# Kernel tuning notes

Hardware: AMD Instinct MI355X
Metric: run time of the kernel (lower is better)

## Reference

```python
import jax, jax.numpy as jnp
import numpy as np

B, A, N_OBS, HX, N_ACT = 8192, 32, 128, 64, 16

def setup_inputs() -> dict:
    key = jax.random.key(0)
    ks = jax.random.split(key, 12)
    s = lambda *shape: 0.05 * jax.random.normal(ks[setup_inputs.i], shape, dtype=jnp.float32)
    out = {}
    setup_inputs.i = 0
    def nxt(*shape):
        setup_inputs.i += 1
        return 0.05 * jax.random.normal(ks[setup_inputs.i], shape, dtype=jnp.float32)
    out['obs'] = jax.random.normal(ks[0], (B, A, N_OBS), dtype=jnp.float32)
    out['W1'] = nxt(A, N_OBS, 128); out['b1'] = nxt(A, 128)
    out['W2'] = nxt(A, 128, HX);   out['b2'] = nxt(A, HX)
    out['Wg'] = nxt(A, HX, 2);     out['bg'] = nxt(A, 2)
    out['Wc'] = nxt(A, 2 * HX, HX); out['bc'] = nxt(A, HX)
    out['Wd'] = nxt(A, HX, N_ACT); out['bd'] = nxt(A, N_ACT)
    out['comm_mask'] = jax.random.randint(jax.random.fold_in(key, 99), (A, A), 0, 2, dtype=jnp.int32)
    return out

def reference(obs, W1, b1, W2, b2, Wg, bg, Wc, bc, Wd, bd, comm_mask):
    # encode: per-agent 2-layer MLP, batched over agents via einsum
    x = jax.nn.relu(jnp.einsum('ban,anh->bah', obs, W1) + b1)      # [B,A,128]
    h = jax.nn.relu(jnp.einsum('bah,ahk->bak', x, W2) + b2)        # [B,A,HX]
    # gate: Linear->ReLU->Softmax (computed as in original; only used via the
    # host-side RNG in the torch code, externalized here as comm_mask)
    gates = jax.nn.softmax(jax.nn.relu(jnp.einsum('bak,akg->bag', h, Wg) + bg), axis=-1)
    # communication: for agent i, mean of hidden states of communicating j != i
    mask = comm_mask.astype(h.dtype) * (1.0 - jnp.eye(A, dtype=h.dtype))  # [A_i, A_j]
    total = jnp.einsum('ij,bjk->bik', mask, h)                      # [B,A,HX]
    count = mask.sum(axis=1)                                        # [A]
    comm = total / jnp.maximum(count, 1.0)[None, :, None]           # count==0 -> zeros
    comm_in = jnp.concatenate([h, comm], axis=-1)                   # [B,A,2*HX]
    h2 = jnp.tanh(jnp.einsum('bac,ack->bak', comm_in, Wc) + bc)     # [B,A,HX]
    q = jnp.einsum('bak,akn->ban', h2, Wd) + bd                     # [B,A,N_ACT]
    return q
```

## Files before the change

### kernel.cpp

```cpp
#include <hip/hip_runtime.h>


#define NB   8192
#define NA   32
#define NOBS 128
#define NH1  128
#define HXX  64
#define NACT 16

typedef _Float16 half8 __attribute__((ext_vector_type(8)));
typedef _Float16 half4 __attribute__((ext_vector_type(4)));
typedef float    floatx4 __attribute__((ext_vector_type(4)));

#define MFMA16(af, bf, c) __builtin_amdgcn_mfma_f32_16x16x32_f16((af), (bf), (c), 0, 0, 0)

#define HWS_OFF 0
#define W1P_OFF (NB * NA * HXX)
#define W1P_CNT (NA * 8 * 4 * 512)
#define W2P_OFF (W1P_OFF + W1P_CNT)
#define W2P_CNT (NA * 4 * 4 * 512)
#define WCP_OFF (W2P_OFF + W2P_CNT)
#define WCP_CNT (NA * 4 * 4 * 512)
#define WDP_OFF (WCP_OFF + WCP_CNT)
#define WDP_CNT (NA * 1 * 2 * 512)
#define MN_OFF  (WDP_OFF + WDP_CNT)
#define PACK_TOTAL (W1P_CNT + W2P_CNT + WCP_CNT + WDP_CNT)

#define HSTR 2056
#define DEC_LDS (16 * HSTR * 2)

__device__ __forceinline__ float fast_tanh(float x) {
    x = fminf(fmaxf(x, -10.f), 10.f);
    float e2 = __expf(2.f * x);
    return (e2 - 1.f) / (e2 + 1.f);
}

extern "C" __global__ void pack_kernel(const float* __restrict__ W1,
                                       const float* __restrict__ W2,
                                       const float* __restrict__ Wc,
                                       const float* __restrict__ Wd,
                                       const int*   __restrict__ cmask,
                                       _Float16* __restrict__ ws)
{
    int e = blockIdx.x * 256 + threadIdx.x;
    if (e >= PACK_TOTAL + NA * NA) return;
    if (e >= PACK_TOTAL) {
        int r = e - PACK_TOTAL, i = r >> 5, j = r & 31;
        int c = 0;
        for (int jj = 0; jj < NA; ++jj) c += (jj != i && cmask[i * NA + jj]) ? 1 : 0;
        float v = 0.f;
        if (j != i && cmask[i * NA + j]) v = 1.0f / (float)(c > 1 ? c : 1);
        ((float*)(ws + MN_OFF))[r] = v;
        return;
    }
    const float* src; _Float16* dst; int K, N, NT, NS, r;
    if (e < W1P_CNT) {
        src = W1; dst = ws + W1P_OFF; K = 128; N = 128; NT = 8; NS = 4; r = e;
    } else if (e < W1P_CNT + W2P_CNT) {
        src = W2; dst = ws + W2P_OFF; K = 128; N = 64; NT = 4; NS = 4; r = e - W1P_CNT;
    } else if (e < W1P_CNT + W2P_CNT + WCP_CNT) {
        src = Wc; dst = ws + WCP_OFF; K = 128; N = 64; NT = 4; NS = 4; r = e - W1P_CNT - W2P_CNT;
    } else {
        src = Wd; dst = ws + WDP_OFF; K = 64; N = 16; NT = 1; NS = 2; r = e - W1P_CNT - W2P_CNT - WCP_CNT;
    }
    int j = r & 7, l = (r >> 3) & 63;
    int rest = r >> 9;
    int s  = rest % NS; rest /= NS;
    int nt = rest % NT; rest /= NT;
    int a  = rest;
    int k = s * 32 + (l >> 4) * 8 + j;
    int n = nt * 16 + (l & 15);
    dst[r] = (_Float16)src[((size_t)a * K + k) * N + n];
}

extern "C" __global__ __launch_bounds__(256)
void enc_kernel(const float* __restrict__ obs,
                const float* __restrict__ b1,
                const float* __restrict__ b2,
                const _Float16* __restrict__ W1p,
                const _Float16* __restrict__ W2p,
                _Float16* __restrict__ hws)
{
    __shared__ _Float16 A[128 * 136];

    const int t  = threadIdx.x;
    const int a  = blockIdx.y;
    const int b0 = blockIdx.x * 128;

    {
        const int j = t & 7;
        #pragma unroll
        for (int p = 0; p < 4; ++p) {
            const int row = (t >> 3) + 32 * p;
            const float4* src = (const float4*)(obs + ((size_t)(b0 + row) * NA + a) * NOBS);
            _Float16* dst = A + row * 136;
            #pragma unroll
            for (int q = 0; q < 4; ++q) {
                float4 g = src[j + 8 * q];
                half4 hv; hv[0] = (_Float16)g.x; hv[1] = (_Float16)g.y;
                hv[2] = (_Float16)g.z; hv[3] = (_Float16)g.w;
                *(half4*)&dst[(j + 8 * q) * 4] = hv;
            }
        }
    }
    const int w = t >> 6, l = t & 63, lm = l & 15, lq = l >> 4;

    float b1v[8], b2v[4];
    #pragma unroll
    for (int nt = 0; nt < 8; ++nt) b1v[nt] = b1[a * NH1 + nt * 16 + lm];
    #pragma unroll
    for (int nt = 0; nt < 4; ++nt) b2v[nt] = b2[a * HXX + nt * 16 + lm];

    __syncthreads();

    floatx4 acc[2][8];
    #pragma unroll
    for (int mt = 0; mt < 2; ++mt)
        #pragma unroll
        for (int nt = 0; nt < 8; ++nt) acc[mt][nt] = (floatx4){0.f, 0.f, 0.f, 0.f};
    for (int s = 0; s < 4; ++s) {
        half8 af[2];
        #pragma unroll
        for (int mt = 0; mt < 2; ++mt)
            af[mt] = *(const half8*)&A[(w * 32 + mt * 16 + lm) * 136 + s * 32 + lq * 8];
        #pragma unroll
        for (int nt = 0; nt < 8; ++nt) {
            half8 bf = *(const half8*)&W1p[(((a * 8 + nt) * 4 + s) * 512) + l * 8];
            acc[0][nt] = MFMA16(af[0], bf, acc[0][nt]);
            acc[1][nt] = MFMA16(af[1], bf, acc[1][nt]);
        }
    }
    #pragma unroll
    for (int mt = 0; mt < 2; ++mt)
        #pragma unroll
        for (int nt = 0; nt < 8; ++nt)
            #pragma unroll
            for (int v = 0; v < 4; ++v) {
                float x = fmaxf(acc[mt][nt][v] + b1v[nt], 0.f);
                A[(w * 32 + mt * 16 + lq * 4 + v) * 136 + nt * 16 + lm] = (_Float16)x;
            }

    floatx4 acc2[2][4];
    #pragma unroll
    for (int mt = 0; mt < 2; ++mt)
        #pragma unroll
        for (int nt = 0; nt < 4; ++nt) acc2[mt][nt] = (floatx4){0.f, 0.f, 0.f, 0.f};
    for (int s = 0; s < 4; ++s) {
        half8 af[2];
        #pragma unroll
        for (int mt = 0; mt < 2; ++mt)
            af[mt] = *(const half8*)&A[(w * 32 + mt * 16 + lm) * 136 + s * 32 + lq * 8];
        #pragma unroll
        for (int nt = 0; nt < 4; ++nt) {
            half8 bf = *(const half8*)&W2p[(((a * 4 + nt) * 4 + s) * 512) + l * 8];
            acc2[0][nt] = MFMA16(af[0], bf, acc2[0][nt]);
            acc2[1][nt] = MFMA16(af[1], bf, acc2[1][nt]);
        }
    }
    #pragma unroll
    for (int mt = 0; mt < 2; ++mt)
        #pragma unroll
        for (int nt = 0; nt < 4; ++nt)
            #pragma unroll
            for (int v = 0; v < 4; ++v) {
                float x = fmaxf(acc2[mt][nt][v] + b2v[nt], 0.f);
                A[(w * 32 + mt * 16 + lq * 4 + v) * 136 + nt * 16 + lm] = (_Float16)x;
            }
    {
        const int rr = l >> 2, cc = l & 3;
        #pragma unroll
        for (int mt = 0; mt < 2; ++mt)
            #pragma unroll
            for (int hh = 0; hh < 2; ++hh) {
                const int chunk = cc + 4 * hh;
                const int row = w * 32 + mt * 16 + rr;
                half8 hv = *(const half8*)&A[row * 136 + chunk * 8];
                *(half8*)&hws[((size_t)(b0 + row) * NA + a) * HXX + chunk * 8] = hv;
            }
    }
}

extern "C" __global__ __launch_bounds__(512)
void dec_kernel(const _Float16* __restrict__ hws,
                const float* __restrict__ MnG,
                const float* __restrict__ bc,
                const float* __restrict__ bd,
                const _Float16* __restrict__ Wcp,
                const _Float16* __restrict__ Wdp,
                float* __restrict__ out)
{
    extern __shared__ char smem[];
    _Float16* H = (_Float16*)smem;

    const int t  = threadIdx.x;
    const int b0 = blockIdx.x * 16;

    {
        const uint4* src = (const uint4*)(hws + (size_t)b0 * NA * HXX);
        #pragma unroll
        for (int it = 0; it < 8; ++it) {
            int idx = it * 512 + t;
            int row = idx >> 8, rem = idx & 255;
            *(uint4*)&H[row * HSTR + rem * 8] = src[idx];
        }
    }
    __syncthreads();

    const int w = t >> 6, l = t & 63, lm = l & 15, lq = l >> 4;

    half8 hacc[4][2];
    #pragma unroll
    for (int g = 0; g < 4; ++g)
        #pragma unroll
        for (int sb = 0; sb < 2; ++sb)
            #pragma unroll
            for (int q = 0; q < 8; ++q) hacc[g][sb][q] = (_Float16)0.f;

    #pragma unroll 4
    for (int j = 0; j < NA; ++j) {
        half8 v0 = *(const half8*)&H[lm * HSTR + j * 64 + lq * 8];
        half8 v1 = *(const half8*)&H[lm * HSTR + j * 64 + 32 + lq * 8];
        #pragma unroll
        for (int g = 0; g < 4; ++g) {
            int ag = __builtin_amdgcn_readfirstlane(w * 4 + g);
            _Float16 mh = (_Float16)MnG[ag * NA + j];
            hacc[g][0] += v0 * mh;
            hacc[g][1] += v1 * mh;
        }
    }
    __syncthreads();

    half4 h2r[4][4];
    #pragma unroll
    for (int nt = 0; nt < 4; ++nt) {
        floatx4 acc[4];
        #pragma unroll
        for (int g = 0; g < 4; ++g) acc[g] = (floatx4){0.f, 0.f, 0.f, 0.f};
        #pragma unroll
        for (int s = 0; s < 4; ++s) {
            #pragma unroll
            for (int g = 0; g < 4; ++g) {
                int ag = w * 4 + g;
                half8 af = (s < 2)
                    ? *(const half8*)&H[lm * HSTR + ag * 64 + s * 32 + lq * 8]
                    : hacc[g][s - 2];
                half8 bf = *(const half8*)&Wcp[(((ag * 4 + nt) * 4 + s) * 512) + l * 8];
                acc[g] = MFMA16(af, bf, acc[g]);
            }
        }
        #pragma unroll
        for (int g = 0; g < 4; ++g) {
            int ag = w * 4 + g;
            float bcv = bc[ag * HXX + nt * 16 + lm];
            #pragma unroll
            for (int v = 0; v < 4; ++v)
                h2r[g][nt][v] = (_Float16)fast_tanh(acc[g][v] + bcv);
        }
    }

    #pragma unroll
    for (int g = 0; g < 4; ++g) {
        int ag = w * 4 + g;
        #pragma unroll
        for (int nt = 0; nt < 4; ++nt)
            #pragma unroll
            for (int v = 0; v < 4; ++v)
                H[(lq * 4 + v) * HSTR + ag * 64 + nt * 16 + lm] = h2r[g][nt][v];
    }

    floatx4 acc3[4];
    #pragma unroll
    for (int g = 0; g < 4; ++g) acc3[g] = (floatx4){0.f, 0.f, 0.f, 0.f};
    #pragma unroll
    for (int s = 0; s < 2; ++s) {
        #pragma unroll
        for (int g = 0; g < 4; ++g) {
            int ag = w * 4 + g;
            half8 af = *(const half8*)&H[lm * HSTR + ag * 64 + s * 32 + lq * 8];
            half8 bf = *(const half8*)&Wdp[((ag * 2 + s) * 512) + l * 8];
            acc3[g] = MFMA16(af, bf, acc3[g]);
        }
    }

    #pragma unroll
    for (int g = 0; g < 4; ++g) {
        int ag = w * 4 + g;
        float bdv = bd[ag * NACT + lm];
        #pragma unroll
        for (int v = 0; v < 4; ++v) {
            int row = lq * 4 + v;
            out[((size_t)(b0 + row) * NA + ag) * NACT + lm] = acc3[g][v] + bdv;
        }
    }
}

extern "C" void kernel_launch(void* const* d_in, const int* in_sizes, int n_in,
                              void* d_out, int out_size, void* d_ws, size_t ws_size,
                              hipStream_t stream)
{
    const float* obs = (const float*)d_in[0];
    const float* W1  = (const float*)d_in[1];
    const float* b1  = (const float*)d_in[2];
    const float* W2  = (const float*)d_in[3];
    const float* b2  = (const float*)d_in[4];
    const float* Wc  = (const float*)d_in[7];
    const float* bc  = (const float*)d_in[8];
    const float* Wd  = (const float*)d_in[9];
    const float* bd  = (const float*)d_in[10];
    const int*   cm  = (const int*)d_in[11];

    float*    outp = (float*)d_out;
    _Float16* ws   = (_Float16*)d_ws;

    _Float16* hws = ws + HWS_OFF;
    _Float16* W1p = ws + W1P_OFF;
    _Float16* W2p = ws + W2P_OFF;
    _Float16* Wcp = ws + WCP_OFF;
    _Float16* Wdp = ws + WDP_OFF;
    const float* MnG = (const float*)(ws + MN_OFF);

    hipLaunchKernelGGL(pack_kernel, dim3((PACK_TOTAL + NA * NA + 255) / 256),
                       dim3(256), 0, stream, W1, W2, Wc, Wd, cm, ws);

    hipLaunchKernelGGL(enc_kernel, dim3(NB / 128, NA), dim3(256), 0, stream,
                       obs, b1, b2, W1p, W2p, hws);

    (void)hipFuncSetAttribute((const void*)dec_kernel,
                              hipFuncAttributeMaxDynamicSharedMemorySize, DEC_LDS);
    hipLaunchKernelGGL(dec_kernel, dim3(NB / 16), dim3(512), DEC_LDS, stream,
                       hws, MnG, bc, bd, Wcp, Wdp, outp);
}
```

Measured before the change: 304.3 us.

## Double-buffer encoder obs loads via async global_load_lds with per-wave tiles

Rewrites the encoder so each wave owns a 16KB LDS slab and streams its 8 row-tiles of 16 rows each. The next tile's fp32 obs is prefetched straight into LDS with global_load_lds, using an XOR swizzle, while the current tile runs its MFMAs. This replaces the synchronous load, convert and __syncthreads staging, so the obs load latency is meant to overlap with compute. Blocks now cover 512 rows and need 64KB of dynamic LDS, which cuts the grid to 16x32 blocks and may limit occupancy. The conversion from fp32 to fp16 now happens on LDS reads, and the hand-written waitcnt counts must exactly match the outstanding loads.

```diff
diff --git a/kernel.cpp b/kernel.cpp
--- a/kernel.cpp
+++ b/kernel.cpp
@@ -28,6 +28,14 @@
 
 #define HSTR 2056
 #define DEC_LDS (16 * HSTR * 2)
+
+#define ENC_ROWS_BLK 512
+#define ENC_TILES    8
+#define ENC_SLAB     16384
+#define ENC_LDS      (4 * ENC_SLAB)
+
+using gas1p = const __attribute__((address_space(1))) void*;
+using las3p = __attribute__((address_space(3))) void*;
 
 __device__ __forceinline__ float fast_tanh(float x) {
     x = fminf(fmaxf(x, -10.f), 10.f);
@@ -73,7 +81,7 @@
     dst[r] = (_Float16)src[((size_t)a * K + k) * N + n];
 }
 
-extern "C" __global__ __launch_bounds__(256)
+extern "C" __global__ __launch_bounds__(256, 2)
 void enc_kernel(const float* __restrict__ obs,
                 const float* __restrict__ b1,
                 const float* __restrict__ b2,
@@ -81,29 +89,17 @@
                 const _Float16* __restrict__ W2p,
                 _Float16* __restrict__ hws)
 {
-    __shared__ _Float16 A[128 * 136];
-
-    const int t  = threadIdx.x;
-    const int a  = blockIdx.y;
-    const int b0 = blockIdx.x * 128;
-
-    {
-        const int j = t & 7;
-        #pragma unroll
-        for (int p = 0; p < 4; ++p) {
-            const int row = (t >> 3) + 32 * p;
-            const float4* src = (const float4*)(obs + ((size_t)(b0 + row) * NA + a) * NOBS);
-            _Float16* dst = A + row * 136;
-            #pragma unroll
-            for (int q = 0; q < 4; ++q) {
-                float4 g = src[j + 8 * q];
-                half4 hv; hv[0] = (_Float16)g.x; hv[1] = (_Float16)g.y;
-                hv[2] = (_Float16)g.z; hv[3] = (_Float16)g.w;
-                *(half4*)&dst[(j + 8 * q) * 4] = hv;
-            }
-        }
-    }
-    const int w = t >> 6, l = t & 63, lm = l & 15, lq = l >> 4;
+    extern __shared__ char smem[];
+
+    const int tid  = threadIdx.x;
+    const int a    = blockIdx.y;
+    const int w    = tid >> 6, l = tid & 63;
+    const int lm   = l & 15, lq = l >> 4;
+    const int hrow = l >> 5;
+    const int cch  = l & 31;
+    char* SB = smem + w * ENC_SLAB;
+
+    const int rowb = blockIdx.x * ENC_ROWS_BLK + w * 16;
 
     float b1v[8], b2v[4];
     #pragma unroll
@@ -111,72 +107,93 @@
     #pragma unroll
     for (int nt = 0; nt < 4; ++nt) b2v[nt] = b2[a * HXX + nt * 16 + lm];
 
-    __syncthreads();
-
-    floatx4 acc[2][8];
-    #pragma unroll
-    for (int mt = 0; mt < 2; ++mt)
-        #pragma unroll
-        for (int nt = 0; nt < 8; ++nt) acc[mt][nt] = (floatx4){0.f, 0.f, 0.f, 0.f};
-    for (int s = 0; s < 4; ++s) {
-        half8 af[2];
-        #pragma unroll
-        for (int mt = 0; mt < 2; ++mt)
-            af[mt] = *(const half8*)&A[(w * 32 + mt * 16 + lm) * 136 + s * 32 + lq * 8];
-        #pragma unroll
-        for (int nt = 0; nt < 8; ++nt) {
-            half8 bf = *(const half8*)&W1p[(((a * 8 + nt) * 4 + s) * 512) + l * 8];
-            acc[0][nt] = MFMA16(af[0], bf, acc[0][nt]);
-            acc[1][nt] = MFMA16(af[1], bf, acc[1][nt]);
-        }
-    }
-    #pragma unroll
-    for (int mt = 0; mt < 2; ++mt)
+    auto issue = [&](int t, int q) {
+        #pragma unroll
+        for (int i = 0; i < 8; ++i) {
+            const int r = 2 * i + hrow;
+            const int g = cch ^ (r & 7);
+            const float* gp = obs + ((size_t)(rowb + t * 64 + r) * NA + a) * NOBS + g * 4;
+            __builtin_amdgcn_global_load_lds((gas1p)gp,
+                                             (las3p)(SB + q * 8192 + i * 1024),
+                                             16, 0, 0);
+        }
+    };
+
+    int p = 0;
+    issue(0, 0);
+
+    #pragma unroll 2
+    for (int t = 0; t < ENC_TILES; ++t) {
+        if (t < ENC_TILES - 1) {
+            asm volatile("s_waitcnt lgkmcnt(0)" ::: "memory");
+            issue(t + 1, p ^ 1);
+            asm volatile("s_waitcnt vmcnt(8)" ::: "memory");
+        } else {
+            asm volatile("s_waitcnt vmcnt(0)" ::: "memory");
+        }
+        __builtin_amdgcn_sched_barrier(0);
+
+        const char* SBp = SB + p * 8192;
+        _Float16*   X   = (_Float16*)(SB + p * 8192);
+        const int   rx  = lm & 7;
+
+        floatx4 acc1[8];
+        #pragma unroll
+        for (int nt = 0; nt < 8; ++nt) acc1[nt] = (floatx4){0.f, 0.f, 0.f, 0.f};
+        #pragma unroll
+        for (int s = 0; s < 4; ++s) {
+            const int c0 = s * 8 + lq * 2;
+            floatx4 f0 = *(const floatx4*)(SBp + lm * 512 + (((c0    ) ^ rx) << 4));
+            floatx4 f1 = *(const floatx4*)(SBp + lm * 512 + (((c0 + 1) ^ rx) << 4));
+            half8 af;
+            af[0] = (_Float16)f0[0]; af[1] = (_Float16)f0[1];
+            af[2] = (_Float16)f0[2]; af[3] = (_Float16)f0[3];
+            af[4] = (_Float16)f1[0]; af[5] = (_Float16)f1[1];
+            af[6] = (_Float16)f1[2]; af[7] = (_Float16)f1[3];
+            #pragma unroll
+            for (int nt = 0; nt < 8; ++nt) {
+                half8 bf = *(const half8*)&W1p[(((a * 8 + nt) * 4 + s) * 512) + l * 8];
+                acc1[nt] = MFMA16(af, bf, acc1[nt]);
+            }
+        }
         #pragma unroll
         for (int nt = 0; nt < 8; ++nt)
             #pragma unroll
             for (int v = 0; v < 4; ++v) {
-                float x = fmaxf(acc[mt][nt][v] + b1v[nt], 0.f);
-                A[(w * 32 + mt * 16 + lq * 4 + v) * 136 + nt * 16 + lm] = (_Float16)x;
-            }
-
-    floatx4 acc2[2][4];
-    #pragma unroll
-    for (int mt = 0; mt < 2; ++mt)
-        #pragma unroll
-        for (int nt = 0; nt < 4; ++nt) acc2[mt][nt] = (floatx4){0.f, 0.f, 0.f, 0.f};
-    for (int s = 0; s < 4; ++s) {
-        half8 af[2];
-        #pragma unroll
-        for (int mt = 0; mt < 2; ++mt)
-            af[mt] = *(const half8*)&A[(w * 32 + mt * 16 + lm) * 136 + s * 32 + lq * 8];
-        #pragma unroll
-        for (int nt = 0; nt < 4; ++nt) {
-            half8 bf = *(const half8*)&W2p[(((a * 4 + nt) * 4 + s) * 512) + l * 8];
-            acc2[0][nt] = MFMA16(af[0], bf, acc2[0][nt]);
-            acc2[1][nt] = MFMA16(af[1], bf, acc2[1][nt]);
-        }
-    }
-    #pragma unroll
-    for (int mt = 0; mt < 2; ++mt)
+                float xv = fmaxf(acc1[nt][v] + b1v[nt], 0.f);
+                X[(lq * 4 + v) * 136 + nt * 16 + lm] = (_Float16)xv;
+            }
+
+        floatx4 acc2[4];
+        #pragma unroll
+        for (int nt = 0; nt < 4; ++nt) acc2[nt] = (floatx4){0.f, 0.f, 0.f, 0.f};
+        #pragma unroll
+        for (int s = 0; s < 4; ++s) {
+            half8 af2 = *(const half8*)&X[lm * 136 + s * 32 + lq * 8];
+            #pragma unroll
+            for (int nt = 0; nt < 4; ++nt) {
+                half8 bf = *(const half8*)&W2p[(((a * 4 + nt) * 4 + s) * 512) + l * 8];
+                acc2[nt] = MFMA16(af2, bf, acc2[nt]);
+            }
+        }
         #pragma unroll
         for (int nt = 0; nt < 4; ++nt)
             #pragma unroll
             for (int v = 0; v < 4; ++v) {
-                float x = fmaxf(acc2[mt][nt][v] + b2v[nt], 0.f);
-                A[(w * 32 + mt * 16 + lq * 4 + v) * 136 + nt * 16 + lm] = (_Float16)x;
-            }
-    {
-        const int rr = l >> 2, cc = l & 3;
-        #pragma unroll
-        for (int mt = 0; mt < 2; ++mt)
-            #pragma unroll
-            for (int hh = 0; hh < 2; ++hh) {
-                const int chunk = cc + 4 * hh;
-                const int row = w * 32 + mt * 16 + rr;
-                half8 hv = *(const half8*)&A[row * 136 + chunk * 8];
-                *(half8*)&hws[((size_t)(b0 + row) * NA + a) * HXX + chunk * 8] = hv;
-            }
+                float hv = fmaxf(acc2[nt][v] + b2v[nt], 0.f);
+                X[(lq * 4 + v) * 136 + nt * 16 + lm] = (_Float16)hv;
+            }
+
+        {
+            const int rr = l >> 2, cc = l & 3;
+            #pragma unroll
+            for (int q2 = 0; q2 < 2; ++q2) {
+                const int chunk = cc + 4 * q2;
+                half8 hv8 = *(const half8*)&X[rr * 136 + chunk * 8];
+                *(half8*)&hws[((size_t)(rowb + t * 64 + rr) * NA + a) * HXX + chunk * 8] = hv8;
+            }
+        }
+        p ^= 1;
     }
 }
 
@@ -322,8 +339,10 @@
     hipLaunchKernelGGL(pack_kernel, dim3((PACK_TOTAL + NA * NA + 255) / 256),
                        dim3(256), 0, stream, W1, W2, Wc, Wd, cm, ws);
 
-    hipLaunchKernelGGL(enc_kernel, dim3(NB / 128, NA), dim3(256), 0, stream,
-                       obs, b1, b2, W1p, W2p, hws);
+    (void)hipFuncSetAttribute((const void*)enc_kernel,
+                              hipFuncAttributeMaxDynamicSharedMemorySize, ENC_LDS);
+    hipLaunchKernelGGL(enc_kernel, dim3(NB / ENC_ROWS_BLK, NA), dim3(256), ENC_LDS,
+                       stream, obs, b1, b2, W1p, W2p, hws);
 
     (void)hipFuncSetAttribute((const void*)dec_kernel,
                               hipFuncAttributeMaxDynamicSharedMemorySize, DEC_LDS);
```

New measurement: 329.9 us. 1.08x slower.
